# Kernel tuning notes

Hardware: AMD Instinct MI355X
Metric: run time of the kernel (lower is better)

## Reference

```python
import jax, jax.numpy as jnp
import numpy as np
import math

B, S, D, H = 2, 2048, 1024, 16
HD = D // H
KL_GAMMA = 0.1
EPS = 1e-10


def setup_inputs() -> dict:
    key = jax.random.key(0)
    ks = jax.random.split(key, 12)
    # positive inputs + positive weights keep scores > 0 so log(mean(scores)) is finite
    query = jax.random.uniform(ks[0], (B, S, D), dtype=jnp.float32)
    k_in = jax.random.uniform(ks[1], (B, S, D), dtype=jnp.float32)
    v_in = jax.random.uniform(ks[2], (B, S, D), dtype=jnp.float32)
    def w(k):
        return jax.random.uniform(k, (D, D), dtype=jnp.float32) * 0.002
    b = jnp.full((D,), 1e-3, dtype=jnp.float32)
    return {
        "query": query, "key": k_in, "value": v_in,
        "Wq": w(ks[3]), "bq": b,
        "Wk": w(ks[4]), "bk": b,
        "Wv": w(ks[5]), "bv": b,
        "Wo": w(ks[6]), "bo": b,
    }


def reference(query, key, value, Wq, bq, Wk, bk, Wv, bv, Wo, bo):
    Bq, Sq, _ = query.shape
    Sk = key.shape[1]
    # projections, split heads: [B, H, S, HD]
    Q = (query @ Wq + bq).reshape(Bq, Sq, H, HD).transpose(0, 2, 1, 3)
    K = (key @ Wk + bk).reshape(Bq, Sk, H, HD).transpose(0, 2, 1, 3)
    V = (value @ Wv + bv).reshape(Bq, Sk, H, HD).transpose(0, 2, 1, 3)
    scores = jnp.einsum("bhqd,bhkd->bhqk", Q, K) / math.sqrt(HD)  # [B,H,Sq,Sk]
    # KL bias: row-mean broadcast over keys, then log
    target = jnp.mean(scores, axis=-1, keepdims=True)  # [B,H,Sq,1]
    scores = scores + KL_GAMMA * jnp.log(target + EPS)
    attn = jax.nn.softmax(scores, axis=-1)
    ctx = jnp.einsum("bhqk,bhkd->bhqd", attn, V)
    ctx = ctx.transpose(0, 2, 1, 3).reshape(Bq, Sq, D)
    return ctx @ Wo + bo
```

## Files before the change

### kernel.cpp

```cpp
#include <hip/hip_runtime.h>
#include <hip/hip_bf16.h>
#include <stdint.h>


#define NB 2
#define NS 2048
#define ND 1024
#define NH 16
#define HD 64

typedef short bf16x8 __attribute__((ext_vector_type(8)));
typedef short bf16x4 __attribute__((ext_vector_type(4)));
typedef float f32x4 __attribute__((ext_vector_type(4)));
typedef float f32x16 __attribute__((ext_vector_type(16)));
typedef unsigned int u32x4 __attribute__((ext_vector_type(4)));

static __device__ __forceinline__ short f2bf(float f) {
    uint32_t u = __builtin_bit_cast(uint32_t, f);
    uint32_t r = (u + 0x7fffu + ((u >> 16) & 1u)) >> 16;
    return (short)(uint16_t)r;
}

static __device__ __forceinline__ unsigned int cvtpk(float lo, float hi) {
    unsigned int r;
    asm("v_cvt_pk_bf16_f32 %0, %1, %2" : "=v"(r) : "v"(lo), "v"(hi));
    return r;
}

#if __has_builtin(__builtin_amdgcn_exp2f)
#define EXP2(x) __builtin_amdgcn_exp2f(x)
#else
#define EXP2(x) exp2f(x)
#endif

static __device__ __forceinline__ void plswap(unsigned& a, unsigned& b) {
#if __has_builtin(__builtin_amdgcn_permlane32_swap)
    auto r = __builtin_amdgcn_permlane32_swap(a, b, false, false);
    a = r[0]; b = r[1];
#else
    const int l = (int)(threadIdx.x & 63);
    unsigned bl = __shfl(b, l & 31);
    unsigned ah = __shfl(a, (l & 31) + 32);
    a = (l < 32) ? a : bl;
    b = (l < 32) ? ah : b;
#endif
}

typedef __attribute__((address_space(1))) const unsigned int glob_u32;
typedef __attribute__((address_space(3))) unsigned int lds_u32;
static __device__ __forceinline__ void gload16(const void* g, void* l) {
    __builtin_amdgcn_global_load_lds((glob_u32*)g, (lds_u32*)l, 16, 0, 0);
}

#define VMW(N) do { asm volatile("s_waitcnt vmcnt(" #N ")" ::: "memory"); \
                    __builtin_amdgcn_sched_barrier(0); } while (0)
#define BAR()  do { __builtin_amdgcn_s_barrier();                          \
                    __builtin_amdgcn_sched_barrier(0); } while (0)

__global__ __launch_bounds__(256) void prep_cast(const float* __restrict__ q,
                                                 const float* __restrict__ k,
                                                 const float* __restrict__ v,
                                                 short* __restrict__ Qo,
                                                 short* __restrict__ Ko,
                                                 short* __restrict__ Vo) {
    const float* src = (blockIdx.z == 0) ? q : (blockIdx.z == 1) ? k : v;
    short* dst = (blockIdx.z == 0) ? Qo : (blockIdx.z == 1) ? Ko : Vo;
    const size_t i = ((size_t)blockIdx.x * 256 + threadIdx.x) * 8;
    f32x4 a = *(const f32x4*)(src + i);
    f32x4 b = *(const f32x4*)(src + i + 4);
    bf16x8 o;
    o[0] = f2bf(a[0]); o[1] = f2bf(a[1]); o[2] = f2bf(a[2]); o[3] = f2bf(a[3]);
    o[4] = f2bf(b[0]); o[5] = f2bf(b[1]); o[6] = f2bf(b[2]); o[7] = f2bf(b[3]);
    *(bf16x8*)(dst + i) = o;
}

__global__ __launch_bounds__(256) void prep_wt(const float* __restrict__ W0,
                                               const float* __restrict__ W1,
                                               const float* __restrict__ W2,
                                               const float* __restrict__ W3,
                                               short* __restrict__ WtAll) {
    __shared__ short tile[32][33];
    const float* W = (blockIdx.z == 0) ? W0 : (blockIdx.z == 1) ? W1
                   : (blockIdx.z == 2) ? W2 : W3;
    short* Wt = WtAll + (size_t)blockIdx.z * (ND * ND);
    const int tx = threadIdx.x & 31;
    const int ty = threadIdx.x >> 5;
    const int k0 = blockIdx.x * 32, n0 = blockIdx.y * 32;
#pragma unroll
    for (int i = 0; i < 4; i++)
        tile[ty + i * 8][tx] = f2bf(W[(size_t)(k0 + ty + i * 8) * ND + n0 + tx]);
    __syncthreads();
#pragma unroll
    for (int i = 0; i < 4; i++)
        Wt[(size_t)(n0 + ty + i * 8) * ND + k0 + tx] = tile[tx][ty + i * 8];
}

static __device__ __forceinline__ void gemm_stage(const char* A, const char* W,
                                                  char* As3, char* Bs3,
                                                  int buf, int tile,
                                                  int gm, int gn, int lin) {
#pragma unroll
    for (int j = 0; j < 2; j++) {
        const int lj = lin + (j << 10);
        const int row = lj >> 6;
        const int colL = (lj & 63) ^ (((row ^ (row >> 2)) & 3) << 4);
        gload16(A + (size_t)(gm + row) * (ND * 2) + tile * 64 + colL,
                As3 + buf * 8192 + lj);
        gload16(W + (size_t)(gn + row) * (ND * 2) + tile * 64 + colL,
                Bs3 + buf * 8192 + lj);
    }
}

static __device__ __forceinline__ void gemm_step(const char* AsB, const char* BsB,
                                                 int wr, int wc, int r, int g,
                                                 f32x4 (&acc)[4][4]) {
    bf16x8 af[4], bfv[4];
#pragma unroll
    for (int m = 0; m < 4; m++) {
        const int ar = wr * 64 + m * 16 + r;
        const int fa = ((ar ^ (ar >> 2)) & 3) << 4;
        af[m] = *(const bf16x8*)(AsB + ar * 64 + ((g << 4) ^ fa));
    }
#pragma unroll
    for (int n = 0; n < 4; n++) {
        const int br = wc * 64 + n * 16 + r;
        const int fb = ((br ^ (br >> 2)) & 3) << 4;
        bfv[n] = *(const bf16x8*)(BsB + br * 64 + ((g << 4) ^ fb));
    }
#pragma unroll
    for (int m = 0; m < 4; m++)
#pragma unroll
        for (int n = 0; n < 4; n++)
            acc[m][n] = __builtin_amdgcn_mfma_f32_16x16x32_bf16(
                af[m], bfv[n], acc[m][n], 0, 0, 0);
}

static __device__ __forceinline__ void gemm_body(const short* __restrict__ A,
                                                 const short* __restrict__ Wt,
                                                 const float* __restrict__ bias,
                                                 void* __restrict__ Out,
                                                 int mode, float scale,
                                                 char* As3, char* Bs3) {
    const int tid = threadIdx.x;
    const int gm = blockIdx.x * 128;
    const int gn = blockIdx.y * 128;
    const int w = tid >> 6;
    const int l = tid & 63;
    const int r = l & 15;
    const int g = l >> 4;
    const int wr = w >> 1, wc = w & 1;
    const char* Ap = (const char*)A;
    const char* Wp = (const char*)Wt;

    f32x4 acc[4][4];
#pragma unroll
    for (int m = 0; m < 4; m++)
#pragma unroll
        for (int n = 0; n < 4; n++) acc[m][n] = (f32x4){0.f, 0.f, 0.f, 0.f};

    const int lin = ((w * 2) << 10) + l * 16;

    gemm_stage(Ap, Wp, As3, Bs3, 0, 0, gm, gn, lin);
    gemm_stage(Ap, Wp, As3, Bs3, 1, 1, gm, gn, lin);

    int cur = 0, stg = 2;
    for (int t = 0; t < ND / 32 - 2; t++) {
        gemm_stage(Ap, Wp, As3, Bs3, stg, t + 2, gm, gn, lin);
        VMW(8);
        BAR();
        gemm_step(As3 + cur * 8192, Bs3 + cur * 8192, wr, wc, r, g, acc);
        BAR();
        cur = (cur == 2) ? 0 : cur + 1;
        stg = (stg == 2) ? 0 : stg + 1;
    }
    VMW(4);
    BAR();
    gemm_step(As3 + cur * 8192, Bs3 + cur * 8192, wr, wc, r, g, acc);
    BAR();
    cur = (cur == 2) ? 0 : cur + 1;
    VMW(0);
    BAR();
    gemm_step(As3 + cur * 8192, Bs3 + cur * 8192, wr, wc, r, g, acc);

#pragma unroll
    for (int m = 0; m < 4; m++) {
        const int orow = gm + wr * 64 + m * 16 + g * 4;
#pragma unroll
        for (int n = 0; n < 4; n++) {
            const int ocol = gn + wc * 64 + n * 16 + r;
            const float bv = bias[ocol];
#pragma unroll
            for (int i = 0; i < 4; i++) {
                const float vout = (acc[m][n][i] + bv) * scale;
                const int row = orow + i;
                if (mode == 0) {
                    const int b = row >> 11, s = row & 2047;
                    const int h = ocol >> 6, hd = ocol & 63;
                    ((short*)Out)[(((size_t)(b * NH + h) * NS + s) << 6) + hd] = f2bf(vout);
                } else if (mode == 1) {
                    const int b = row >> 11, s = row & 2047;
                    const int h = ocol >> 6, hd = ocol & 63;
                    ((short*)Out)[((size_t)(b * NH + h) * HD + hd) * NS + s] = f2bf(vout);
                } else {
                    ((float*)Out)[(size_t)row * ND + ocol] = vout;
                }
            }
        }
    }
}

#define QSCALE 0.18033688011112042f

__global__ __launch_bounds__(256, 3) void gemm_qkv(const short* __restrict__ Qin,
                                                   const short* __restrict__ Kin,
                                                   const short* __restrict__ Vin,
                                                   const short* __restrict__ WtAll,
                                                   const float* __restrict__ bq,
                                                   const float* __restrict__ bk,
                                                   const float* __restrict__ bv,
                                                   short* __restrict__ Qo,
                                                   short* __restrict__ Ko,
                                                   short* __restrict__ Vto) {
    __shared__ __align__(16) char As[3 * 8192];
    __shared__ __align__(16) char Bs[3 * 8192];
    const int z = blockIdx.z;
    const short* A = (z == 0) ? Qin : (z == 1) ? Kin : Vin;
    const short* Wt = WtAll + (size_t)z * ND * ND;
    const float* bias = (z == 0) ? bq : (z == 1) ? bk : bv;
    void* Out = (z == 0) ? (void*)Qo : (z == 1) ? (void*)Ko : (void*)Vto;
    const float scale = (z == 0) ? QSCALE : 1.0f;
    const int mode = (z == 2) ? 1 : 0;
    gemm_body(A, Wt, bias, Out, mode, scale, As, Bs);
}

__global__ __launch_bounds__(256, 3) void gemm_fin(const short* __restrict__ Ctx,
                                                   const short* __restrict__ Wt,
                                                   const float* __restrict__ bo,
                                                   float* __restrict__ Out) {
    __shared__ __align__(16) char As[3 * 8192];
    __shared__ __align__(16) char Bs[3 * 8192];
    gemm_body(Ctx, Wt, bo, Out, 2, 1.0f, As, Bs);
}

static __device__ __forceinline__ void stage2(const char* Kp8, const char* Vp8,
                                              char* Kbuf, char* Vbuf,
                                              int t, int w, int l) {
#pragma unroll
    for (int jj = 0; jj < 2; jj++) {
        const int chunk = w * 2 + jj;
        const int half = chunk >> 3;
        const int lin = ((chunk & 7) << 10) + l * 16;
        const int sw = lin ^ (((lin >> 7) & 7) << 4);
        const int row = sw >> 7, col = sw & 127;
        gload16(Kp8 + (size_t)(half * 1024 + t * 64 + row) * 128 + col,
                Kbuf + half * 8192 + ((chunk & 7) << 10));
        gload16(Vp8 + (size_t)row * (NS * 2) + (half * 1024 + t * 64) * 2 + col,
                Vbuf + half * 8192 + ((chunk & 7) << 10));
    }
}

__global__ __launch_bounds__(512, 2) void attn_kern(const short* __restrict__ Q,
                                                    const short* __restrict__ K,
                                                    const short* __restrict__ Vt,
                                                    short* __restrict__ Ctx) {
    __shared__ __align__(16) char smem[2][2][16384];
    __shared__ float rsbuf[8][2][32];

    const int tid = threadIdx.x;
    const int w = tid >> 6;
    const int l = tid & 63;
    const int c = l & 31;
    const int h = l >> 5;
    const int h16 = h << 4;

    const int bid = blockIdx.x;
    const int swb = (bid & 7) * 32 + (bid >> 3);
    const int bh = swb >> 3;
    const int qt = swb & 7;
    const int g = w & 3;
    const int khalf = w >> 2;
    const int qw = qt * 256 + g * 64;

    const short* Qp = Q + (size_t)bh * NS * HD;
    const char* Kp8 = (const char*)(K + (size_t)bh * NS * HD);
    const char* Vp8 = (const char*)(Vt + (size_t)bh * HD * NS);

    bf16x8 qf[2][4];
#pragma unroll
    for (int qc = 0; qc < 2; qc++)
#pragma unroll
        for (int st = 0; st < 4; st++)
            qf[qc][st] = *(const bf16x8*)(Qp + (size_t)(qw + qc * 32 + c) * HD +
                                          st * 16 + h * 8);

    f32x16 acc[2][2];
#pragma unroll
    for (int qc = 0; qc < 2; qc++)
#pragma unroll
        for (int dt = 0; dt < 2; dt++) acc[qc][dt] = (f32x16)(0.f);
    float rs0 = 0.f, rs1 = 0.f;

    const int sx = (c & 7) << 4;

    stage2(Kp8, Vp8, smem[0][0], smem[0][1], 0, w, l);

    int bufi = 0;
#pragma unroll 1
    for (int t = 0; t < 16; t++) {
        if (t < 15) {
            stage2(Kp8, Vp8, smem[bufi ^ 1][0], smem[bufi ^ 1][1], t + 1, w, l);
            VMW(4);
        } else {
            VMW(0);
        }
        BAR();

        const char* Kt = smem[bufi][0] + khalf * 8192;
        const char* Vv = smem[bufi][1] + khalf * 8192;

#pragma unroll
        for (int ktile = 0; ktile < 2; ktile++) {
            bf16x8 kf[4];
#pragma unroll
            for (int st = 0; st < 4; st++)
                kf[st] = *(const bf16x8*)(Kt + ((ktile * 32 + c) << 7) +
                                          ((st * 32 + h16) ^ sx));
            f32x16 S0 = (f32x16)(0.f), S1 = (f32x16)(0.f);
#pragma unroll
            for (int st = 0; st < 4; st++) {
                S0 = __builtin_amdgcn_mfma_f32_32x32x16_bf16(kf[st], qf[0][st], S0, 0, 0, 0);
                S1 = __builtin_amdgcn_mfma_f32_32x32x16_bf16(kf[st], qf[1][st], S1, 0, 0, 0);
            }

            float tv0[16], tv1[16];
#pragma unroll
            for (int i = 0; i < 16; i++) {
                tv0[i] = EXP2(S0[i]); rs0 += tv0[i];
                tv1[i] = EXP2(S1[i]); rs1 += tv1[i];
            }
            unsigned p0a[4], p0b[4], p1a[4], p1b[4];
#pragma unroll
            for (int q4 = 0; q4 < 4; q4++) {
                p0a[q4] = cvtpk(tv0[4 * q4], tv0[4 * q4 + 1]);
                p0b[q4] = cvtpk(tv0[4 * q4 + 2], tv0[4 * q4 + 3]);
                p1a[q4] = cvtpk(tv1[4 * q4], tv1[4 * q4 + 1]);
                p1b[q4] = cvtpk(tv1[4 * q4 + 2], tv1[4 * q4 + 3]);
            }

#pragma unroll
            for (int ks = 0; ks < 2; ks++) {
                unsigned a0 = p0a[2 * ks], b0 = p0a[2 * ks + 1];
                unsigned a1 = p0b[2 * ks], b1 = p0b[2 * ks + 1];
                plswap(a0, b0); plswap(a1, b1);
                u32x4 pw0; pw0[0] = a0; pw0[1] = a1; pw0[2] = b0; pw0[3] = b1;
                bf16x8 pa0 = __builtin_bit_cast(bf16x8, pw0);
                unsigned c0 = p1a[2 * ks], d0 = p1a[2 * ks + 1];
                unsigned c1 = p1b[2 * ks], d1 = p1b[2 * ks + 1];
                plswap(c0, d0); plswap(c1, d1);
                u32x4 pw1; pw1[0] = c0; pw1[1] = c1; pw1[2] = d0; pw1[3] = d1;
                bf16x8 pa1 = __builtin_bit_cast(bf16x8, pw1);
#pragma unroll
                for (int dt = 0; dt < 2; dt++) {
                    bf16x8 vb = *(const bf16x8*)(Vv + ((dt * 32 + c) << 7) +
                                                 ((ktile * 64 + ks * 32 + h16) ^ sx));
                    acc[0][dt] = __builtin_amdgcn_mfma_f32_32x32x16_bf16(pa0, vb, acc[0][dt], 0, 0, 0);
                    acc[1][dt] = __builtin_amdgcn_mfma_f32_32x32x16_bf16(pa1, vb, acc[1][dt], 0, 0, 0);
                }
            }
        }
        BAR();
        bufi ^= 1;
    }

    rs0 += __shfl_xor(rs0, 32);
    rs1 += __shfl_xor(rs1, 32);
    if (h == 0) { rsbuf[w][0][c] = rs0; rsbuf[w][1][c] = rs1; }

    float* sumbuf = (float*)&smem[0][0][0];
    if (w >= 4) {
#pragma unroll
        for (int qc = 0; qc < 2; qc++)
#pragma unroll
            for (int q4 = 0; q4 < 4; q4++)
#pragma unroll
                for (int i = 0; i < 4; i++) {
                    const int qrow = qc * 32 + i + 8 * q4 + 4 * h;
#pragma unroll
                    for (int dt = 0; dt < 2; dt++)
                        sumbuf[((g * 64 + qrow) << 6) + dt * 32 + c] =
                            acc[qc][dt][q4 * 4 + i];
                }
    }
    __syncthreads();
    if (w < 4) {
        const int b = bh >> 4, hh = bh & 15;
#pragma unroll
        for (int qc = 0; qc < 2; qc++)
#pragma unroll
            for (int q4 = 0; q4 < 4; q4++)
#pragma unroll
                for (int i = 0; i < 4; i++) {
                    const int qrow32 = i + 8 * q4 + 4 * h;
                    const int qrow = qc * 32 + qrow32;
                    const float inv = 1.0f / (rsbuf[g][qc][qrow32] +
                                              rsbuf[4 + g][qc][qrow32]);
                    short* op = Ctx + ((size_t)b * NS + qt * 256 + g * 64 + qrow) * ND +
                                hh * HD;
#pragma unroll
                    for (int dt = 0; dt < 2; dt++) {
                        const float val = acc[qc][dt][q4 * 4 + i] +
                                          sumbuf[((g * 64 + qrow) << 6) + dt * 32 + c];
                        op[dt * 32 + c] = f2bf(val * inv);
                    }
                }
    }
}

extern "C" void kernel_launch(void* const* d_in, const int* in_sizes, int n_in,
                              void* d_out, int out_size, void* d_ws, size_t ws_size,
                              hipStream_t stream) {
    (void)in_sizes; (void)n_in; (void)out_size; (void)ws_size;
    const float* query = (const float*)d_in[0];
    const float* key_  = (const float*)d_in[1];
    const float* value = (const float*)d_in[2];
    const float* Wq = (const float*)d_in[3];
    const float* bq = (const float*)d_in[4];
    const float* Wk = (const float*)d_in[5];
    const float* bk = (const float*)d_in[6];
    const float* Wv = (const float*)d_in[7];
    const float* bv = (const float*)d_in[8];
    const float* Wo = (const float*)d_in[9];
    const float* bo = (const float*)d_in[10];

    char* ws = (char*)d_ws;
    const size_t MB = 1024 * 1024;
    short* WtAll = (short*)ws;
    short* Qin = (short*)(ws + 8 * MB);
    short* Kin = (short*)(ws + 16 * MB);
    short* Vin = (short*)(ws + 24 * MB);
    short* Qb  = (short*)(ws + 32 * MB);
    short* Kb  = (short*)(ws + 40 * MB);
    short* Vtb = (short*)(ws + 48 * MB);
    short* Ctx = (short*)(ws + 8 * MB);

    prep_cast<<<dim3(2048, 1, 3), 256, 0, stream>>>(query, key_, value, Qin, Kin, Vin);
    prep_wt<<<dim3(32, 32, 4), 256, 0, stream>>>(Wq, Wk, Wv, Wo, WtAll);
    gemm_qkv<<<dim3(32, 8, 3), 256, 0, stream>>>(Qin, Kin, Vin, WtAll, bq, bk, bv,
                                                 Qb, Kb, Vtb);
    attn_kern<<<dim3(256), 512, 0, stream>>>(Qb, Kb, Vtb, Ctx);
    gemm_fin<<<dim3(32, 8), 256, 0, stream>>>(Ctx, WtAll + 3 * ND * ND, bo, (float*)d_out);
}
```

Measured before the change: 118.2 us.

## Fuse fp32-to-bf16 input cast into QKV GEMM via register-prefetched A operand

Removes the separate prep_cast kernel and has gemm_qkv read fp32 activations straight from global memory into registers, converting them to bf16 just before the MFMAs. Only the weight tiles are staged through LDS with the triple buffer, while the A fragments are double-buffered in registers. gemm_fin uses the same register-prefetch scheme for its bf16 Ctx operand. This saves a full read/write pass over the inputs and one launch. In exchange the A loads are less coalesced, since they are per-lane row loads that are not shared through LDS, and register pressure rises.

```diff
diff --git a/kernel.cpp b/kernel.cpp
--- a/kernel.cpp
+++ b/kernel.cpp
@@ -56,23 +56,7 @@
                     __builtin_amdgcn_sched_barrier(0); } while (0)
 #define BAR()  do { __builtin_amdgcn_s_barrier();                          \
                     __builtin_amdgcn_sched_barrier(0); } while (0)
-
-__global__ __launch_bounds__(256) void prep_cast(const float* __restrict__ q,
-                                                 const float* __restrict__ k,
-                                                 const float* __restrict__ v,
-                                                 short* __restrict__ Qo,
-                                                 short* __restrict__ Ko,
-                                                 short* __restrict__ Vo) {
-    const float* src = (blockIdx.z == 0) ? q : (blockIdx.z == 1) ? k : v;
-    short* dst = (blockIdx.z == 0) ? Qo : (blockIdx.z == 1) ? Ko : Vo;
-    const size_t i = ((size_t)blockIdx.x * 256 + threadIdx.x) * 8;
-    f32x4 a = *(const f32x4*)(src + i);
-    f32x4 b = *(const f32x4*)(src + i + 4);
-    bf16x8 o;
-    o[0] = f2bf(a[0]); o[1] = f2bf(a[1]); o[2] = f2bf(a[2]); o[3] = f2bf(a[3]);
-    o[4] = f2bf(b[0]); o[5] = f2bf(b[1]); o[6] = f2bf(b[2]); o[7] = f2bf(b[3]);
-    *(bf16x8*)(dst + i) = o;
-}
+#define SFENCE() __builtin_amdgcn_sched_barrier(0)
 
 __global__ __launch_bounds__(256) void prep_wt(const float* __restrict__ W0,
                                                const float* __restrict__ W1,
@@ -95,52 +79,86 @@
         Wt[(size_t)(n0 + ty + i * 8) * ND + k0 + tx] = tile[tx][ty + i * 8];
 }
 
-static __device__ __forceinline__ void gemm_stage(const char* A, const char* W,
-                                                  char* As3, char* Bs3,
-                                                  int buf, int tile,
-                                                  int gm, int gn, int lin) {
-#pragma unroll
-    for (int j = 0; j < 2; j++) {
-        const int lj = lin + (j << 10);
-        const int row = lj >> 6;
-        const int colL = (lj & 63) ^ (((row ^ (row >> 2)) & 3) << 4);
-        gload16(A + (size_t)(gm + row) * (ND * 2) + tile * 64 + colL,
-                As3 + buf * 8192 + lj);
-        gload16(W + (size_t)(gn + row) * (ND * 2) + tile * 64 + colL,
-                Bs3 + buf * 8192 + lj);
-    }
-}
-
-static __device__ __forceinline__ void gemm_step(const char* AsB, const char* BsB,
-                                                 int wr, int wc, int r, int g,
-                                                 f32x4 (&acc)[4][4]) {
-    bf16x8 af[4], bfv[4];
-#pragma unroll
-    for (int m = 0; m < 4; m++) {
-        const int ar = wr * 64 + m * 16 + r;
-        const int fa = ((ar ^ (ar >> 2)) & 3) << 4;
-        af[m] = *(const bf16x8*)(AsB + ar * 64 + ((g << 4) ^ fa));
-    }
-#pragma unroll
-    for (int n = 0; n < 4; n++) {
-        const int br = wc * 64 + n * 16 + r;
-        const int fb = ((br ^ (br >> 2)) & 3) << 4;
-        bfv[n] = *(const bf16x8*)(BsB + br * 64 + ((g << 4) ^ fb));
-    }
-#pragma unroll
-    for (int m = 0; m < 4; m++)
-#pragma unroll
-        for (int n = 0; n < 4; n++)
-            acc[m][n] = __builtin_amdgcn_mfma_f32_16x16x32_bf16(
-                af[m], bfv[n], acc[m][n], 0, 0, 0);
-}
-
-static __device__ __forceinline__ void gemm_body(const short* __restrict__ A,
-                                                 const short* __restrict__ Wt,
-                                                 const float* __restrict__ bias,
-                                                 void* __restrict__ Out,
-                                                 int mode, float scale,
-                                                 char* As3, char* Bs3) {
+#define QSCALE 0.18033688011112042f
+
+
+#define BSTAGE(slot, t)                                                       \
+  { _Pragma("unroll") for (int j = 0; j < 2; j++) {                           \
+      const int lj = (j << 12) + tid * 16;                                    \
+      const int brow = lj >> 6;                                               \
+      const int colL = (lj & 63) ^ (((brow ^ (brow >> 2)) & 3) << 4);         \
+      gload16(Wp + (size_t)(gn + brow) * (ND * 2) + (t) * 64 + colL,          \
+              Bs + (slot) * 8192 + lj);                                       \
+    } SFENCE(); }
+
+#define APF_F32(PN, t)                                                        \
+  { _Pragma("unroll") for (int m = 0; m < 4; m++) {                           \
+      const float* ap = Af + (size_t)(m * 16) * ND + (t) * 32 + g * 8;        \
+      PN[2 * m]     = *(const f32x4*)(ap);                                    \
+      PN[2 * m + 1] = *(const f32x4*)(ap + 4);                                \
+    } SFENCE(); }
+
+#define APF_BF16(PN, t)                                                       \
+  { _Pragma("unroll") for (int m = 0; m < 4; m++)                             \
+      PN[m] = *(const bf16x8*)(Ab + (size_t)(m * 16) * ND + (t) * 32 + g * 8);\
+    SFENCE(); }
+
+#define QCOMP(PC, bc)                                                         \
+  { bf16x8 af[4], bfv[4];                                                     \
+    _Pragma("unroll") for (int m = 0; m < 4; m++) {                           \
+      u32x4 t_;                                                               \
+      t_[0] = cvtpk(PC[2 * m][0], PC[2 * m][1]);                              \
+      t_[1] = cvtpk(PC[2 * m][2], PC[2 * m][3]);                              \
+      t_[2] = cvtpk(PC[2 * m + 1][0], PC[2 * m + 1][1]);                      \
+      t_[3] = cvtpk(PC[2 * m + 1][2], PC[2 * m + 1][3]);                      \
+      af[m] = __builtin_bit_cast(bf16x8, t_);                                 \
+    }                                                                         \
+    _Pragma("unroll") for (int n = 0; n < 4; n++) {                           \
+      const int br = wc * 64 + n * 16 + r;                                    \
+      const int fb = ((br ^ (br >> 2)) & 3) << 4;                             \
+      bfv[n] = *(const bf16x8*)(Bs + (bc) * 8192 + br * 64 + ((g << 4) ^ fb));\
+    }                                                                         \
+    __builtin_amdgcn_s_setprio(1);                                            \
+    _Pragma("unroll") for (int m = 0; m < 4; m++)                             \
+      _Pragma("unroll") for (int n = 0; n < 4; n++)                           \
+        acc[m][n] = __builtin_amdgcn_mfma_f32_16x16x32_bf16(                  \
+            af[m], bfv[n], acc[m][n], 0, 0, 0);                               \
+    __builtin_amdgcn_s_setprio(0); }
+
+#define FCOMP(PC, bc)                                                         \
+  { bf16x8 bfv[4];                                                            \
+    _Pragma("unroll") for (int n = 0; n < 4; n++) {                           \
+      const int br = wc * 64 + n * 16 + r;                                    \
+      const int fb = ((br ^ (br >> 2)) & 3) << 4;                             \
+      bfv[n] = *(const bf16x8*)(Bs + (bc) * 8192 + br * 64 + ((g << 4) ^ fb));\
+    }                                                                         \
+    __builtin_amdgcn_s_setprio(1);                                            \
+    _Pragma("unroll") for (int m = 0; m < 4; m++)                             \
+      _Pragma("unroll") for (int n = 0; n < 4; n++)                           \
+        acc[m][n] = __builtin_amdgcn_mfma_f32_16x16x32_bf16(                  \
+            PC[m], bfv[n], acc[m][n], 0, 0, 0);                               \
+    __builtin_amdgcn_s_setprio(0); }
+
+__global__ __launch_bounds__(256, 3) void gemm_qkv(const float* __restrict__ Qin,
+                                                   const float* __restrict__ Kin,
+                                                   const float* __restrict__ Vin,
+                                                   const short* __restrict__ WtAll,
+                                                   const float* __restrict__ bq,
+                                                   const float* __restrict__ bk,
+                                                   const float* __restrict__ bv,
+                                                   short* __restrict__ Qo,
+                                                   short* __restrict__ Ko,
+                                                   short* __restrict__ Vto) {
+    __shared__ __align__(16) char Bs[3 * 8192];
+
+    const int z = blockIdx.z;
+    const float* A = (z == 0) ? Qin : (z == 1) ? Kin : Vin;
+    const char* Wp = (const char*)(WtAll + (size_t)z * ND * ND);
+    const float* bias = (z == 0) ? bq : (z == 1) ? bk : bv;
+    const float scale = (z == 0) ? QSCALE : 1.0f;
+    const int mode = (z == 2) ? 1 : 0;
+    void* Out = (z == 0) ? (void*)Qo : (z == 1) ? (void*)Ko : (void*)Vto;
+
     const int tid = threadIdx.x;
     const int gm = blockIdx.x * 128;
     const int gn = blockIdx.y * 128;
@@ -149,8 +167,7 @@
     const int r = l & 15;
     const int g = l >> 4;
     const int wr = w >> 1, wc = w & 1;
-    const char* Ap = (const char*)A;
-    const char* Wp = (const char*)Wt;
+    const float* Af = A + (size_t)(gm + wr * 64 + r) * ND;
 
     f32x4 acc[4][4];
 #pragma unroll
@@ -158,29 +175,28 @@
 #pragma unroll
         for (int n = 0; n < 4; n++) acc[m][n] = (f32x4){0.f, 0.f, 0.f, 0.f};
 
-    const int lin = ((w * 2) << 10) + l * 16;
-
-    gemm_stage(Ap, Wp, As3, Bs3, 0, 0, gm, gn, lin);
-    gemm_stage(Ap, Wp, As3, Bs3, 1, 1, gm, gn, lin);
-
-    int cur = 0, stg = 2;
-    for (int t = 0; t < ND / 32 - 2; t++) {
-        gemm_stage(Ap, Wp, As3, Bs3, stg, t + 2, gm, gn, lin);
-        VMW(8);
-        BAR();
-        gemm_step(As3 + cur * 8192, Bs3 + cur * 8192, wr, wc, r, g, acc);
-        BAR();
-        cur = (cur == 2) ? 0 : cur + 1;
-        stg = (stg == 2) ? 0 : stg + 1;
-    }
-    VMW(4);
-    BAR();
-    gemm_step(As3 + cur * 8192, Bs3 + cur * 8192, wr, wc, r, g, acc);
-    BAR();
-    cur = (cur == 2) ? 0 : cur + 1;
-    VMW(0);
-    BAR();
-    gemm_step(As3 + cur * 8192, Bs3 + cur * 8192, wr, wc, r, g, acc);
+    f32x4 pA[8], pB[8];
+
+    APF_F32(pA, 0);
+    BSTAGE(0, 0);
+    BSTAGE(1, 1);
+
+#define QSTEP(t, PC, PN, DO_ST, VW)                                           \
+  { APF_F32(PN, (t) + 1);                                                     \
+    if (DO_ST) BSTAGE(bst, (t) + 2);                                          \
+    VW; BAR();                                                                \
+    QCOMP(PC, bc);                                                            \
+    BAR();                                                                    \
+    bc = (bc == 2) ? 0 : bc + 1; bst = (bst == 2) ? 0 : bst + 1; }
+
+    int bc = 0, bst = 2;
+    for (int tt = 0; tt < 15; tt++) {
+        QSTEP(2 * tt,     pA, pB, 1, VMW(12));
+        QSTEP(2 * tt + 1, pB, pA, 1, VMW(12));
+    }
+    { APF_F32(pB, 31); VMW(10); BAR(); QCOMP(pA, bc); BAR();
+      bc = (bc == 2) ? 0 : bc + 1; }
+    { VMW(0); BAR(); QCOMP(pB, bc); }
 
 #pragma unroll
     for (int m = 0; m < 4; m++) {
@@ -193,53 +209,75 @@
             for (int i = 0; i < 4; i++) {
                 const float vout = (acc[m][n][i] + bv) * scale;
                 const int row = orow + i;
-                if (mode == 0) {
-                    const int b = row >> 11, s = row & 2047;
-                    const int h = ocol >> 6, hd = ocol & 63;
+                const int b = row >> 11, s = row & 2047;
+                const int h = ocol >> 6, hd = ocol & 63;
+                if (mode == 0)
                     ((short*)Out)[(((size_t)(b * NH + h) * NS + s) << 6) + hd] = f2bf(vout);
-                } else if (mode == 1) {
-                    const int b = row >> 11, s = row & 2047;
-                    const int h = ocol >> 6, hd = ocol & 63;
+                else
                     ((short*)Out)[((size_t)(b * NH + h) * HD + hd) * NS + s] = f2bf(vout);
-                } else {
-                    ((float*)Out)[(size_t)row * ND + ocol] = vout;
-                }
             }
         }
     }
 }
 
-#define QSCALE 0.18033688011112042f
-
-__global__ __launch_bounds__(256, 3) void gemm_qkv(const short* __restrict__ Qin,
-                                                   const short* __restrict__ Kin,
-                                                   const short* __restrict__ Vin,
+__global__ __launch_bounds__(256, 3) void gemm_fin(const short* __restrict__ Ctx,
                                                    const short* __restrict__ WtAll,
-                                                   const float* __restrict__ bq,
-                                                   const float* __restrict__ bk,
-                                                   const float* __restrict__ bv,
-                                                   short* __restrict__ Qo,
-                                                   short* __restrict__ Ko,
-                                                   short* __restrict__ Vto) {
-    __shared__ __align__(16) char As[3 * 8192];
-    __shared__ __align__(16) char Bs[3 * 8192];
-    const int z = blockIdx.z;
-    const short* A = (z == 0) ? Qin : (z == 1) ? Kin : Vin;
-    const short* Wt = WtAll + (size_t)z * ND * ND;
-    const float* bias = (z == 0) ? bq : (z == 1) ? bk : bv;
-    void* Out = (z == 0) ? (void*)Qo : (z == 1) ? (void*)Ko : (void*)Vto;
-    const float scale = (z == 0) ? QSCALE : 1.0f;
-    const int mode = (z == 2) ? 1 : 0;
-    gemm_body(A, Wt, bias, Out, mode, scale, As, Bs);
-}
-
-__global__ __launch_bounds__(256, 3) void gemm_fin(const short* __restrict__ Ctx,
-                                                   const short* __restrict__ Wt,
                                                    const float* __restrict__ bo,
                                                    float* __restrict__ Out) {
-    __shared__ __align__(16) char As[3 * 8192];
     __shared__ __align__(16) char Bs[3 * 8192];
-    gemm_body(Ctx, Wt, bo, Out, 2, 1.0f, As, Bs);
+
+    const char* Wp = (const char*)(WtAll + (size_t)3 * ND * ND);
+    const int tid = threadIdx.x;
+    const int gm = blockIdx.x * 128;
+    const int gn = blockIdx.y * 128;
+    const int w = tid >> 6;
+    const int l = tid & 63;
+    const int r = l & 15;
+    const int g = l >> 4;
+    const int wr = w >> 1, wc = w & 1;
+    const short* Ab = Ctx + (size_t)(gm + wr * 64 + r) * ND;
+
+    f32x4 acc[4][4];
+#pragma unroll
+    for (int m = 0; m < 4; m++)
+#pragma unroll
+        for (int n = 0; n < 4; n++) acc[m][n] = (f32x4){0.f, 0.f, 0.f, 0.f};
+
+    bf16x8 pA[4], pB[4];
+
+    APF_BF16(pA, 0);
+    BSTAGE(0, 0);
+    BSTAGE(1, 1);
+
+#define FSTEP(t, PC, PN, DO_ST, VW)                                           \
+  { APF_BF16(PN, (t) + 1);                                                    \
+    if (DO_ST) BSTAGE(bst, (t) + 2);                                          \
+    VW; BAR();                                                                \
+    FCOMP(PC, bc);                                                            \
+    BAR();                                                                    \
+    bc = (bc == 2) ? 0 : bc + 1; bst = (bst == 2) ? 0 : bst + 1; }
+
+    int bc = 0, bst = 2;
+    for (int tt = 0; tt < 15; tt++) {
+        FSTEP(2 * tt,     pA, pB, 1, VMW(8));
+        FSTEP(2 * tt + 1, pB, pA, 1, VMW(8));
+    }
+    { APF_BF16(pB, 31); VMW(6); BAR(); FCOMP(pA, bc); BAR();
+      bc = (bc == 2) ? 0 : bc + 1; }
+    { VMW(0); BAR(); FCOMP(pB, bc); }
+
+#pragma unroll
+    for (int m = 0; m < 4; m++) {
+        const int orow = gm + wr * 64 + m * 16 + g * 4;
+#pragma unroll
+        for (int n = 0; n < 4; n++) {
+            const int ocol = gn + wc * 64 + n * 16 + r;
+            const float bv = bo[ocol];
+#pragma unroll
+            for (int i = 0; i < 4; i++)
+                Out[(size_t)(orow + i) * ND + ocol] = acc[m][n][i] + bv;
+        }
+    }
 }
 
 static __device__ __forceinline__ void stage2(const char* Kp8, const char* Vp8,
@@ -435,18 +473,14 @@
     char* ws = (char*)d_ws;
     const size_t MB = 1024 * 1024;
     short* WtAll = (short*)ws;
-    short* Qin = (short*)(ws + 8 * MB);
-    short* Kin = (short*)(ws + 16 * MB);
-    short* Vin = (short*)(ws + 24 * MB);
     short* Qb  = (short*)(ws + 32 * MB);
     short* Kb  = (short*)(ws + 40 * MB);
     short* Vtb = (short*)(ws + 48 * MB);
     short* Ctx = (short*)(ws + 8 * MB);
 
-    prep_cast<<<dim3(2048, 1, 3), 256, 0, stream>>>(query, key_, value, Qin, Kin, Vin);
     prep_wt<<<dim3(32, 32, 4), 256, 0, stream>>>(Wq, Wk, Wv, Wo, WtAll);
-    gemm_qkv<<<dim3(32, 8, 3), 256, 0, stream>>>(Qin, Kin, Vin, WtAll, bq, bk, bv,
-                                                 Qb, Kb, Vtb);
+    gemm_qkv<<<dim3(32, 8, 3), 256, 0, stream>>>(query, key_, value, WtAll,
+                                                 bq, bk, bv, Qb, Kb, Vtb);
     attn_kern<<<dim3(256), 512, 0, stream>>>(Qb, Kb, Vtb, Ctx);
-    gemm_fin<<<dim3(32, 8), 256, 0, stream>>>(Ctx, WtAll + 3 * ND * ND, bo, (float*)d_out);
-}
+    gemm_fin<<<dim3(32, 8), 256, 0, stream>>>(Ctx, WtAll, bo, (float*)d_out);
+}
```

Result: slower. 178.6 us (+51.1%).
